# Kernel tuning notes

Hardware: AMD Instinct MI355X
Metric: run time of the kernel (lower is better)

Reference implementation:

```python
import jax, jax.numpy as jnp
import numpy as np

B, S, D, H, K = 8, 1024, 512, 512, 8  # batch, seq, input_dim, hidden, max neighbors


def setup_inputs() -> dict:
    key = jax.random.key(0)
    ks = jax.random.split(key, 10)
    p = lambda k, shape: (0.05 * jax.random.normal(k, shape, jnp.float32))
    return {
        "input_t": jax.random.normal(ks[0], (B, S, D), jnp.float32),
        "comb_idx": jax.random.randint(ks[1], (B, S, K), 0, S, jnp.int32),
        "comb_mask": jax.random.randint(ks[2], (B, S, K), 0, 2, jnp.int32),
        "order": jnp.arange(B, dtype=jnp.int64),
        # PyTorch LSTM params per direction; b = b_ih + b_hh fused (mathematically identical)
        "w_ih_f": p(ks[3], (4 * H, D)),
        "w_hh_f": p(ks[4], (4 * H, H)),
        "b_f": p(ks[5], (4 * H,)),
        "w_ih_b": p(ks[6], (4 * H, D)),
        "w_hh_b": p(ks[7], (4 * H, H)),
        "b_b": p(ks[8], (4 * H,)),
    }


def _lstm_scan(x_sbd, w_ih, w_hh, b, reverse):
    # x_sbd: [S, B, D]; PyTorch gate order i, f, g, o; zero initial state (inithidden)
    Bb = x_sbd.shape[1]
    Hh = w_hh.shape[1]
    h0 = jnp.zeros((Bb, Hh), x_sbd.dtype)
    c0 = jnp.zeros((Bb, Hh), x_sbd.dtype)

    def cell(carry, xt):
        h, c = carry
        z = xt @ w_ih.T + h @ w_hh.T + b
        i, f, g, o = jnp.split(z, 4, axis=-1)
        c = jax.nn.sigmoid(f) * c + jax.nn.sigmoid(i) * jnp.tanh(g)
        h = jax.nn.sigmoid(o) * jnp.tanh(c)
        return (h, c), h

    (hn, cn), hs = jax.lax.scan(cell, (h0, c0), x_sbd, reverse=reverse)
    return hs, hn, cn  # hs in original time order even when reverse=True


def reference(input_t, comb_idx, comb_mask, order, w_ih_f, w_hh_f, b_f, w_ih_b, w_hh_b, b_b):
    x = jnp.swapaxes(input_t, 0, 1)  # [S, B, D]
    hs_f, hn_f, cn_f = _lstm_scan(x, w_ih_f, w_hh_f, b_f, reverse=False)
    hs_b, hn_b, cn_b = _lstm_scan(x, w_ih_b, w_hh_b, b_b, reverse=True)
    padded = jnp.swapaxes(jnp.concatenate([hs_f, hs_b], axis=-1), 0, 1)  # [B, S, 2H]
    h_n = jnp.stack([hn_f, hn_b])  # [2, B, H]
    c_n = jnp.stack([cn_f, cn_b])

    # comb = batch_comb[order[idx]]
    ci = comb_idx[order]                                  # [B, S, K]
    cm = comb_mask[order].astype(padded.dtype)            # [B, S, K]
    gathered = jax.vmap(lambda xb, ib: xb[ib])(padded, ci)  # [B, S, K, 2H]
    neigh_sum = (gathered * cm[..., None]).sum(axis=2)    # [B, S, 2H]
    cnt = cm.sum(axis=-1)                                 # [B, S]
    rep = (padded + neigh_sum) / (1.0 + cnt)[..., None]   # (x_i + sum_j x_j) / (|comb_i| + 1)
    rep = rep[:, 1:-1, :]                                 # drop first/last token

    # reorder_batch_encoder_rep[order[i]] = rep[i]
    out = jnp.zeros_like(rep).at[order].set(rep)
    return out, h_n, c_n
```

## Files before the change

kernel.cpp:

```cpp
#include <hip/hip_runtime.h>
#include <stdint.h>

typedef unsigned short u16;
typedef unsigned long long u64;
typedef __attribute__((ext_vector_type(8))) short short8v;
typedef __attribute__((ext_vector_type(4))) float f32x4;

#define OUT_HN   8372224
#define OUT_CN   8380416

#define WS_FLAGS 0
#define WS_CSB   4096
#define WS_HSB0  36864
#define WS_HSB1  8433664
#define WS_ZX    16830464

__device__ __forceinline__ u16 f2bf(float f) {
  uint32_t u = __float_as_uint(f);
  u += 0x7FFFu + ((u >> 16) & 1u);
  return (u16)(u >> 16);
}
__device__ __forceinline__ float bf2f(u16 v) {
  return __uint_as_float(((uint32_t)v) << 16);
}
__device__ __forceinline__ short8v cvt8(const float* p) {
  float4 a = *(const float4*)p;
  float4 b = *(const float4*)(p + 4);
  short8v r;
  r[0] = (short)f2bf(a.x); r[1] = (short)f2bf(a.y);
  r[2] = (short)f2bf(a.z); r[3] = (short)f2bf(a.w);
  r[4] = (short)f2bf(b.x); r[5] = (short)f2bf(b.y);
  r[6] = (short)f2bf(b.z); r[7] = (short)f2bf(b.w);
  return r;
}

__global__ void k_init(uint32_t* flags) {
  if (threadIdx.x < 64) flags[threadIdx.x] = 0;
}

__global__ void k_zero(u16* h0, u16* h1, float* c) {
  int i = blockIdx.x * blockDim.x + threadIdx.x;
  if (i < 4096) { h0[i] = 0; h1[i] = 0; }
  if (i < 8192) c[i] = 0.f;
}

#define STAGE_X(tcol)                                                          \
  {                                                                            \
    _Pragma("unroll")                                                          \
    for (int half = 0; half < 2; ++half) {                                     \
      int g = tid + half * 256;                                                \
      int r = g >> 6, B = g & 63;                                              \
      const float* xr = xf + ((size_t)r * 1024 + (tcol)) * 512 + B * 8;        \
      float4 a = *(const float4*)xr;                                           \
      float4 b = *(const float4*)(xr + 4);                                     \
      short8v v;                                                               \
      v[0] = (short)f2bf(a.x); v[1] = (short)f2bf(a.y);                        \
      v[2] = (short)f2bf(a.z); v[3] = (short)f2bf(a.w);                        \
      v[4] = (short)f2bf(b.x); v[5] = (short)f2bf(b.y);                        \
      v[6] = (short)f2bf(b.z); v[7] = (short)f2bf(b.w);                        \
      *(short8v*)(xL + r * 512 + ((B ^ r) << 3)) = v;                          \
    }                                                                          \
  }

__global__ void k_zx(const float* __restrict__ xf,
                     const float* __restrict__ wihf, const float* __restrict__ wihb,
                     u16* __restrict__ zx, int s0, int seglen)
{
  const int nch  = seglen >> 5;
  const int bid  = blockIdx.x;
  const int chunk = bid % nch;
  const int wg   = (bid / nch) & 15;
  const int dir  = bid / (nch * 16);
  const int tid  = threadIdx.x;
  const int wid  = tid >> 6;
  const int lane = tid & 63;
  const int jbase = wg * 32;
  const float* wih = dir ? wihb : wihf;

  __shared__ u16 xL[8 * 512];
  __shared__ float zL[4 * 8 * 32];

  short8v bih[2][16];
  {
    const int rr = lane & 15;
    const int ko = (lane >> 4) * 8;
    #pragma unroll
    for (int nt = 0; nt < 2; ++nt) {
      const int row = wid * 512 + jbase + nt * 16 + rr;
      #pragma unroll
      for (int kt = 0; kt < 16; ++kt)
        bih[nt][kt] = cvt8(wih + (size_t)row * 512 + kt * 32 + ko);
    }
  }

  const int rB = lane & 7;
  const int q  = lane >> 4;
  const f32x4 fzero = {0.f, 0.f, 0.f, 0.f};

  for (int i = 0; i < 32; ++i) {
    const int sidx = chunk * 32 + i;
    const int gstep = s0 + sidx;
    const int tn = dir ? (1023 - gstep) : gstep;
    STAGE_X(tn);
    __syncthreads();
    f32x4 acc0 = fzero, acc1 = fzero;
    #pragma unroll
    for (int kt = 0; kt < 16; ++kt) {
      short8v ax = *(const short8v*)(xL + rB * 512 + (((kt * 4 + q) ^ rB) << 3));
      acc0 = __builtin_amdgcn_mfma_f32_16x16x32_bf16(ax, bih[0][kt], acc0, 0, 0, 0);
      acc1 = __builtin_amdgcn_mfma_f32_16x16x32_bf16(ax, bih[1][kt], acc1, 0, 0, 0);
    }
    if (lane < 32) {
      #pragma unroll
      for (int r = 0; r < 4; ++r) {
        const int brow = (lane >> 4) * 4 + r;
        zL[wid * 256 + brow * 32 + (lane & 15)]      = acc0[r];
        zL[wid * 256 + brow * 32 + 16 + (lane & 15)] = acc1[r];
      }
    }
    __syncthreads();
    if (tid < 128) {
      const int b = tid >> 4;
      const int r = (tid & 15) * 8;
      const int g = r >> 5;
      const int jj = r & 31;
      short8v v;
      #pragma unroll
      for (int w = 0; w < 8; ++w) v[w] = (short)f2bf(zL[g * 256 + b * 32 + jj + w]);
      *(short8v*)(zx + (((size_t)dir * seglen + sidx) * 16 + wg) * 1024 + tid * 8) = v;
    }
    __syncthreads();
  }
}

__launch_bounds__(256, 1)
__global__ void k_lstm(const float* __restrict__ whhf, const float* __restrict__ whhb,
                       const float* __restrict__ bias0, const float* __restrict__ bias1,
                       const u16* __restrict__ zx,
                       u16* hsb0, u16* hsb1, float* csb, float* out,
                       uint32_t* flags, int s0, int s1, int seglen)
{
  const int tid  = threadIdx.x;
  const int wid  = tid >> 6;
  const int lane = tid & 63;
  const int dir  = blockIdx.x >> 4;
  const int wg   = blockIdx.x & 15;
  const int jbase = wg * 32;

  const float* whh  = dir ? whhb : whhf;
  const float* bias = dir ? bias1 : bias0;
  u16* hsb = dir ? hsb1 : hsb0;
  uint32_t* fl = flags + dir * 16;

  __shared__ u16 hL[8 * 512];
  __shared__ float zL[4 * 8 * 32];
  __shared__ u16 hS[8 * 32];
  __shared__ u64 zxL[256];

  short8v bhh[2][16];
  {
    const int rr = lane & 15;
    const int ko = (lane >> 4) * 8;
    #pragma unroll
    for (int nt = 0; nt < 2; ++nt) {
      const int row = wid * 512 + jbase + nt * 16 + rr;
      #pragma unroll
      for (int kt = 0; kt < 16; ++kt)
        bhh[nt][kt] = cvt8(whh + (size_t)row * 512 + kt * 32 + ko);
    }
  }

  const int cb = tid >> 5;
  const int cj = tid & 31;
  const float bz0 = bias[0 * 512 + jbase + cj];
  const float bz1 = bias[1 * 512 + jbase + cj];
  const float bz2 = bias[2 * 512 + jbase + cj];
  const float bz3 = bias[3 * 512 + jbase + cj];
  float* cp = csb + dir * 4096 + cb * 512 + jbase + cj;
  float c_state = *cp;

  const int rB = lane & 7;
  const int q  = lane >> 4;
  const f32x4 fzero = {0.f, 0.f, 0.f, 0.f};
  const u16* zx16 = (const u16*)zxL;

  for (int gstep = s0; gstep < s1; ++gstep) {
    {
      const u64* zp = (const u64*)(zx + (((size_t)dir * seglen + (gstep - s0)) * 16 + wg) * 1024);
      zxL[tid] = zp[tid];
    }
    if (tid < 16) {
      int guard = 0;
      while (__hip_atomic_load(&fl[tid], __ATOMIC_RELAXED, __HIP_MEMORY_SCOPE_AGENT)
             < (uint32_t)gstep && ++guard < (1 << 15)) { }
    }
    __syncthreads();
    {
      const u64* hc = (const u64*)(hsb + (size_t)gstep * 4096);
      u64 d0 = __hip_atomic_load(hc + 4 * tid + 0, __ATOMIC_RELAXED, __HIP_MEMORY_SCOPE_AGENT);
      u64 d1 = __hip_atomic_load(hc + 4 * tid + 1, __ATOMIC_RELAXED, __HIP_MEMORY_SCOPE_AGENT);
      u64 d2 = __hip_atomic_load(hc + 4 * tid + 2, __ATOMIC_RELAXED, __HIP_MEMORY_SCOPE_AGENT);
      u64 d3 = __hip_atomic_load(hc + 4 * tid + 3, __ATOMIC_RELAXED, __HIP_MEMORY_SCOPE_AGENT);
      union { u64 qq[2]; short8v v; } p0, p1;
      p0.qq[0] = d0; p0.qq[1] = d1;
      p1.qq[0] = d2; p1.qq[1] = d3;
      int G0 = 2 * tid, G1 = 2 * tid + 1;
      int r0 = G0 >> 6, B0 = G0 & 63;
      int r1 = G1 >> 6, B1 = G1 & 63;
      *(short8v*)(hL + r0 * 512 + ((B0 ^ r0) << 3)) = p0.v;
      *(short8v*)(hL + r1 * 512 + ((B1 ^ r1) << 3)) = p1.v;
    }
    __syncthreads();
    f32x4 acc0 = fzero, acc1 = fzero;
    #pragma unroll
    for (int kt = 0; kt < 16; ++kt) {
      short8v ah = *(const short8v*)(hL + rB * 512 + (((kt * 4 + q) ^ rB) << 3));
      acc0 = __builtin_amdgcn_mfma_f32_16x16x32_bf16(ah, bhh[0][kt], acc0, 0, 0, 0);
      acc1 = __builtin_amdgcn_mfma_f32_16x16x32_bf16(ah, bhh[1][kt], acc1, 0, 0, 0);
    }
    if (lane < 32) {
      #pragma unroll
      for (int r = 0; r < 4; ++r) {
        const int brow = (lane >> 4) * 4 + r;
        zL[wid * 256 + brow * 32 + (lane & 15)]      = acc0[r];
        zL[wid * 256 + brow * 32 + 16 + (lane & 15)] = acc1[r];
      }
    }
    __syncthreads();
    {
      float zi = zL[0 * 256 + cb * 32 + cj] + bz0 + bf2f(zx16[cb * 128 +  0 + cj]);
      float zf = zL[1 * 256 + cb * 32 + cj] + bz1 + bf2f(zx16[cb * 128 + 32 + cj]);
      float zg = zL[2 * 256 + cb * 32 + cj] + bz2 + bf2f(zx16[cb * 128 + 64 + cj]);
      float zo = zL[3 * 256 + cb * 32 + cj] + bz3 + bf2f(zx16[cb * 128 + 96 + cj]);
      float si = 1.f / (1.f + __expf(-zi));
      float sf = 1.f / (1.f + __expf(-zf));
      float so = 1.f / (1.f + __expf(-zo));
      float ag = fabsf(zg); float eg = __expf(-2.f * ag);
      float tg = (1.f - eg) / (1.f + eg); tg = copysignf(tg, zg);
      c_state = sf * c_state + si * tg;
      float ac = fabsf(c_state); float ec = __expf(-2.f * ac);
      float tc = (1.f - ec) / (1.f + ec); tc = copysignf(tc, c_state);
      float h = so * tc;
      hS[cb * 32 + cj] = f2bf(h);
      if (gstep == 1023) {
        out[OUT_HN + dir * 4096 + cb * 512 + jbase + cj] = h;
        out[OUT_CN + dir * 4096 + cb * 512 + jbase + cj] = c_state;
      }
    }
    __syncthreads();
    if (tid < 64) {
      const int pb = tid >> 3;
      const int pt = tid & 7;
      u64 hv = *(const u64*)(hS + pb * 32 + 4 * pt);
      u64* dst = (u64*)(hsb + ((size_t)(gstep + 1) * 8 + pb) * 512 + jbase + 4 * pt);
      __hip_atomic_store(dst, hv, __ATOMIC_RELAXED, __HIP_MEMORY_SCOPE_AGENT);
      asm volatile("s_waitcnt vmcnt(0)" ::: "memory");
    }
    if (tid == 0) {
      __hip_atomic_store(&fl[wg], (uint32_t)(gstep + 1), __ATOMIC_RELAXED,
                         __HIP_MEMORY_SCOPE_AGENT);
    }
  }
  *cp = c_state;
}

__global__ void k_combine(const u16* __restrict__ hsb0, const u16* __restrict__ hsb1,
                          const int* __restrict__ cidx, const int* __restrict__ cmask,
                          const int* __restrict__ order, float* __restrict__ out)
{
  const int tid = threadIdx.x;
  const int b = blockIdx.x / 1022;
  const int s = 1 + (blockIdx.x % 1022);
  __shared__ int sidx[8];
  __shared__ float smask[8];
  __shared__ int rsh;
  if (tid == 0) rsh = order[b];
  __syncthreads();
  const int r = rsh;
  if (tid < 8) {
    size_t base = ((size_t)r * 1024 + s) * 8 + tid;
    sidx[tid] = cidx[base];
    smask[tid] = (float)cmask[base];
  }
  __syncthreads();
  float cnt = 0.f;
  #pragma unroll
  for (int k = 0; k < 8; ++k) cnt += smask[k];
  const float inv = 1.f / (1.f + cnt);

  const int col0 = tid * 4;
  const bool isF = col0 < 512;
  const int cloc = isF ? col0 : col0 - 512;
  const u16* hb = isF ? hsb0 : hsb1;

  float v0, v1, v2, v3;
  {
    size_t ci2 = isF ? (size_t)(s + 1) : (size_t)(1024 - s);
    ushort4 qv = *(const ushort4*)(hb + (ci2 * 8 + b) * 512 + cloc);
    v0 = bf2f(qv.x); v1 = bf2f(qv.y); v2 = bf2f(qv.z); v3 = bf2f(qv.w);
  }
  #pragma unroll
  for (int k = 0; k < 8; ++k) {
    float m = smask[k];
    if (m != 0.f) {
      int sp = sidx[k];
      size_t ci2 = isF ? (size_t)(sp + 1) : (size_t)(1024 - sp);
      ushort4 qv = *(const ushort4*)(hb + (ci2 * 8 + b) * 512 + cloc);
      v0 += m * bf2f(qv.x); v1 += m * bf2f(qv.y); v2 += m * bf2f(qv.z); v3 += m * bf2f(qv.w);
    }
  }
  size_t ob = ((size_t)r * 1022 + (s - 1)) * 1024 + col0;
  float4 ov; ov.x = v0 * inv; ov.y = v1 * inv; ov.z = v2 * inv; ov.w = v3 * inv;
  *(float4*)(out + ob) = ov;
}

extern "C" void kernel_launch(void* const* d_in, const int* in_sizes, int n_in,
                              void* d_out, int out_size, void* d_ws, size_t ws_size,
                              hipStream_t stream)
{
  const float* x      = (const float*)d_in[0];
  const int*   cidx   = (const int*)d_in[1];
  const int*   cmask  = (const int*)d_in[2];
  const int*   order  = (const int*)d_in[3];
  const float* wihf = (const float*)d_in[4];
  const float* whhf = (const float*)d_in[5];
  const float* bf   = (const float*)d_in[6];
  const float* wihb = (const float*)d_in[7];
  const float* whhb = (const float*)d_in[8];
  const float* bb   = (const float*)d_in[9];
  float* out = (float*)d_out;

  char* ws = (char*)d_ws;
  uint32_t* FLAGS = (uint32_t*)(ws + WS_FLAGS);
  float* CSB = (float*)(ws + WS_CSB);
  u16* HSB0 = (u16*)(ws + WS_HSB0);
  u16* HSB1 = (u16*)(ws + WS_HSB1);
  u16* ZX   = (u16*)(ws + WS_ZX);

  const int seglen = (ws_size >= (size_t)WS_ZX + 1024ull * 65536) ? 1024 : 128;

  hipLaunchKernelGGL(k_init, dim3(1), dim3(64), 0, stream, FLAGS);
  hipLaunchKernelGGL(k_zero, dim3(32), dim3(256), 0, stream, HSB0, HSB1, CSB);

  for (int s0 = 0; s0 < 1024; s0 += seglen) {
    hipLaunchKernelGGL(k_zx, dim3(2 * 16 * (seglen >> 5)), dim3(256), 0, stream,
                       x, wihf, wihb, ZX, s0, seglen);
    hipLaunchKernelGGL(k_lstm, dim3(32), dim3(256), 0, stream,
                       whhf, whhb, bf, bb, ZX, HSB0, HSB1, CSB, out, FLAGS,
                       s0, s0 + seglen, seglen);
  }

  hipLaunchKernelGGL(k_combine, dim3(8 * 1022), dim3(256), 0, stream,
                     HSB0, HSB1, cidx, cmask, order, out);
}
```

Baseline: 2.974 ms.

## Use a single atomic step counter and load hidden state directly into registers

Replaces the 16 per-workgroup step flags with one shared counter per direction. Each workgroup increments it after publishing its slice of h, and one thread polls until it reaches 16*gstep. The MFMA A-fragments of h are now loaded straight from global memory into registers instead of being staged through a swizzled LDS buffer, which removes one __syncthreads per step. The bf16 MFMA chain is split into even/odd accumulators for more instruction-level parallelism, and the zx prefetch and h publish are moved to different waves. The cost is atomic contention on a single counter and uncoalesced, scattered global loads of h on every step.

```diff
diff --git a/kernel.cpp b/kernel.cpp
--- a/kernel.cpp
+++ b/kernel.cpp
@@ -150,9 +150,8 @@
   const float* whh  = dir ? whhb : whhf;
   const float* bias = dir ? bias1 : bias0;
   u16* hsb = dir ? hsb1 : hsb0;
-  uint32_t* fl = flags + dir * 16;
-
-  __shared__ u16 hL[8 * 512];
+  uint32_t* cnt = flags + dir * 16;
+
   __shared__ float zL[4 * 8 * 32];
   __shared__ u16 hS[8 * 32];
   __shared__ u64 zxL[256];
@@ -185,39 +184,41 @@
   const u16* zx16 = (const u16*)zxL;
 
   for (int gstep = s0; gstep < s1; ++gstep) {
+    if (wid >= 2) {
+      const int t2 = tid - 128;
+      const u64* zp = (const u64*)(zx + (((size_t)dir * seglen + (gstep - s0)) * 16 + wg) * 1024);
+      zxL[2 * t2]     = zp[2 * t2];
+      zxL[2 * t2 + 1] = zp[2 * t2 + 1];
+    }
+    if (tid == 0) {
+      int guard = 0;
+      while (__hip_atomic_load(cnt, __ATOMIC_RELAXED, __HIP_MEMORY_SCOPE_AGENT)
+             < 16u * (uint32_t)gstep && ++guard < (1 << 16)) { }
+    }
+    __syncthreads();
+    short8v hfrag[16];
     {
-      const u64* zp = (const u64*)(zx + (((size_t)dir * seglen + (gstep - s0)) * 16 + wg) * 1024);
-      zxL[tid] = zp[tid];
-    }
-    if (tid < 16) {
-      int guard = 0;
-      while (__hip_atomic_load(&fl[tid], __ATOMIC_RELAXED, __HIP_MEMORY_SCOPE_AGENT)
-             < (uint32_t)gstep && ++guard < (1 << 15)) { }
-    }
-    __syncthreads();
-    {
-      const u64* hc = (const u64*)(hsb + (size_t)gstep * 4096);
-      u64 d0 = __hip_atomic_load(hc + 4 * tid + 0, __ATOMIC_RELAXED, __HIP_MEMORY_SCOPE_AGENT);
-      u64 d1 = __hip_atomic_load(hc + 4 * tid + 1, __ATOMIC_RELAXED, __HIP_MEMORY_SCOPE_AGENT);
-      u64 d2 = __hip_atomic_load(hc + 4 * tid + 2, __ATOMIC_RELAXED, __HIP_MEMORY_SCOPE_AGENT);
-      u64 d3 = __hip_atomic_load(hc + 4 * tid + 3, __ATOMIC_RELAXED, __HIP_MEMORY_SCOPE_AGENT);
-      union { u64 qq[2]; short8v v; } p0, p1;
-      p0.qq[0] = d0; p0.qq[1] = d1;
-      p1.qq[0] = d2; p1.qq[1] = d3;
-      int G0 = 2 * tid, G1 = 2 * tid + 1;
-      int r0 = G0 >> 6, B0 = G0 & 63;
-      int r1 = G1 >> 6, B1 = G1 & 63;
-      *(short8v*)(hL + r0 * 512 + ((B0 ^ r0) << 3)) = p0.v;
-      *(short8v*)(hL + r1 * 512 + ((B1 ^ r1) << 3)) = p1.v;
-    }
-    __syncthreads();
-    f32x4 acc0 = fzero, acc1 = fzero;
+      const char* colbase = (const char*)(hsb + (size_t)gstep * 4096);
+      #pragma unroll
+      for (int kt = 0; kt < 16; ++kt) {
+        const u64* p = (const u64*)(colbase + ((rB * 512 + kt * 32 + q * 8) * 2));
+        u64 lo = __hip_atomic_load(p,     __ATOMIC_RELAXED, __HIP_MEMORY_SCOPE_AGENT);
+        u64 hi = __hip_atomic_load(p + 1, __ATOMIC_RELAXED, __HIP_MEMORY_SCOPE_AGENT);
+        union { u64 q2[2]; short8v v; } u;
+        u.q2[0] = lo; u.q2[1] = hi;
+        hfrag[kt] = u.v;
+      }
+    }
+    f32x4 a0e = fzero, a0o = fzero, a1e = fzero, a1o = fzero;
     #pragma unroll
-    for (int kt = 0; kt < 16; ++kt) {
-      short8v ah = *(const short8v*)(hL + rB * 512 + (((kt * 4 + q) ^ rB) << 3));
-      acc0 = __builtin_amdgcn_mfma_f32_16x16x32_bf16(ah, bhh[0][kt], acc0, 0, 0, 0);
-      acc1 = __builtin_amdgcn_mfma_f32_16x16x32_bf16(ah, bhh[1][kt], acc1, 0, 0, 0);
-    }
+    for (int kt = 0; kt < 16; kt += 2) {
+      a0e = __builtin_amdgcn_mfma_f32_16x16x32_bf16(hfrag[kt],     bhh[0][kt],     a0e, 0, 0, 0);
+      a1e = __builtin_amdgcn_mfma_f32_16x16x32_bf16(hfrag[kt],     bhh[1][kt],     a1e, 0, 0, 0);
+      a0o = __builtin_amdgcn_mfma_f32_16x16x32_bf16(hfrag[kt + 1], bhh[0][kt + 1], a0o, 0, 0, 0);
+      a1o = __builtin_amdgcn_mfma_f32_16x16x32_bf16(hfrag[kt + 1], bhh[1][kt + 1], a1o, 0, 0, 0);
+    }
+    f32x4 acc0 = a0e + a0o;
+    f32x4 acc1 = a1e + a1o;
     if (lane < 32) {
       #pragma unroll
       for (int r = 0; r < 4; ++r) {
@@ -248,17 +249,16 @@
       }
     }
     __syncthreads();
-    if (tid < 64) {
-      const int pb = tid >> 3;
-      const int pt = tid & 7;
+    if (wid == 1) {
+      const int t = tid - 64;
+      const int pb = t >> 3;
+      const int pt = t & 7;
       u64 hv = *(const u64*)(hS + pb * 32 + 4 * pt);
       u64* dst = (u64*)(hsb + ((size_t)(gstep + 1) * 8 + pb) * 512 + jbase + 4 * pt);
       __hip_atomic_store(dst, hv, __ATOMIC_RELAXED, __HIP_MEMORY_SCOPE_AGENT);
       asm volatile("s_waitcnt vmcnt(0)" ::: "memory");
-    }
-    if (tid == 0) {
-      __hip_atomic_store(&fl[wg], (uint32_t)(gstep + 1), __ATOMIC_RELAXED,
-                         __HIP_MEMORY_SCOPE_AGENT);
+      if (t == 0)
+        __hip_atomic_fetch_add(cnt, 1u, __ATOMIC_RELAXED, __HIP_MEMORY_SCOPE_AGENT);
     }
   }
   *cp = c_state;
```

Result: slower. 6.151 ms (+106.8%).

## Split MFMA accumulator chains and spread per-step duties across waves

Applied to the files above, without the earlier changes.

In the recurrent LSTM step loop, the h·W_hh MFMA chain now uses two independent accumulators per output tile (even and odd k-tiles), summed at the end, which shortens the serial dependency chain on each step. The per-step load of the input-projection slice now runs on waves 2–3 only, and publishing h plus the step flag moves from wave 0 to wave 1. Wave 0 then does only the flag spin-wait, so that wait is no longer delayed by unrelated memory traffic. The cost is a few extra vector adds and a slightly different floating-point summation order.

```diff
diff --git a/kernel.cpp b/kernel.cpp
--- a/kernel.cpp
+++ b/kernel.cpp
@@ -185,9 +185,11 @@
   const u16* zx16 = (const u16*)zxL;
 
   for (int gstep = s0; gstep < s1; ++gstep) {
-    {
+    if (wid >= 2) {
+      const int t2 = tid - 128;
       const u64* zp = (const u64*)(zx + (((size_t)dir * seglen + (gstep - s0)) * 16 + wg) * 1024);
-      zxL[tid] = zp[tid];
+      zxL[2 * t2]     = zp[2 * t2];
+      zxL[2 * t2 + 1] = zp[2 * t2 + 1];
     }
     if (tid < 16) {
       int guard = 0;
@@ -211,13 +213,18 @@
       *(short8v*)(hL + r1 * 512 + ((B1 ^ r1) << 3)) = p1.v;
     }
     __syncthreads();
-    f32x4 acc0 = fzero, acc1 = fzero;
+    f32x4 a0e = fzero, a0o = fzero, a1e = fzero, a1o = fzero;
     #pragma unroll
-    for (int kt = 0; kt < 16; ++kt) {
-      short8v ah = *(const short8v*)(hL + rB * 512 + (((kt * 4 + q) ^ rB) << 3));
-      acc0 = __builtin_amdgcn_mfma_f32_16x16x32_bf16(ah, bhh[0][kt], acc0, 0, 0, 0);
-      acc1 = __builtin_amdgcn_mfma_f32_16x16x32_bf16(ah, bhh[1][kt], acc1, 0, 0, 0);
-    }
+    for (int kt = 0; kt < 16; kt += 2) {
+      short8v he = *(const short8v*)(hL + rB * 512 + ((((kt)     * 4 + q) ^ rB) << 3));
+      short8v ho = *(const short8v*)(hL + rB * 512 + ((((kt + 1) * 4 + q) ^ rB) << 3));
+      a0e = __builtin_amdgcn_mfma_f32_16x16x32_bf16(he, bhh[0][kt],     a0e, 0, 0, 0);
+      a1e = __builtin_amdgcn_mfma_f32_16x16x32_bf16(he, bhh[1][kt],     a1e, 0, 0, 0);
+      a0o = __builtin_amdgcn_mfma_f32_16x16x32_bf16(ho, bhh[0][kt + 1], a0o, 0, 0, 0);
+      a1o = __builtin_amdgcn_mfma_f32_16x16x32_bf16(ho, bhh[1][kt + 1], a1o, 0, 0, 0);
+    }
+    f32x4 acc0 = a0e + a0o;
+    f32x4 acc1 = a1e + a1o;
     if (lane < 32) {
       #pragma unroll
       for (int r = 0; r < 4; ++r) {
@@ -248,17 +255,17 @@
       }
     }
     __syncthreads();
-    if (tid < 64) {
-      const int pb = tid >> 3;
-      const int pt = tid & 7;
+    if (wid == 1) {
+      const int t = tid - 64;
+      const int pb = t >> 3;
+      const int pt = t & 7;
       u64 hv = *(const u64*)(hS + pb * 32 + 4 * pt);
       u64* dst = (u64*)(hsb + ((size_t)(gstep + 1) * 8 + pb) * 512 + jbase + 4 * pt);
       __hip_atomic_store(dst, hv, __ATOMIC_RELAXED, __HIP_MEMORY_SCOPE_AGENT);
       asm volatile("s_waitcnt vmcnt(0)" ::: "memory");
-    }
-    if (tid == 0) {
-      __hip_atomic_store(&fl[wg], (uint32_t)(gstep + 1), __ATOMIC_RELAXED,
-                         __HIP_MEMORY_SCOPE_AGENT);
+      if (t == 0)
+        __hip_atomic_store(&fl[wg], (uint32_t)(gstep + 1), __ATOMIC_RELAXED,
+                           __HIP_MEMORY_SCOPE_AGENT);
     }
   }
   *cp = c_state;
```

Result: slower. 3.198 ms (+7.5%).

## Halve LSTM recurrence workgroups to 16 with 512 threads each

Applied to the files above, without the earlier changes.

The persistent recurrent LSTM kernel now uses 8 workgroups per direction, each of 512 threads covering 64 hidden units, instead of 16 workgroups of 256 threads covering 32 units. Each step therefore has fewer cross-workgroup flags to poll and fewer participants in the global handoff of h, which targets the per-step synchronisation latency that dominates the sequential scan. In exchange each workgroup does twice the gate math per step and holds more LDS, and only 16 CUs take part in the recurrence.

```diff
diff --git a/kernel.cpp b/kernel.cpp
--- a/kernel.cpp
+++ b/kernel.cpp
@@ -133,7 +133,7 @@
   }
 }
 
-__launch_bounds__(256, 1)
+__launch_bounds__(512, 1)
 __global__ void k_lstm(const float* __restrict__ whhf, const float* __restrict__ whhb,
                        const float* __restrict__ bias0, const float* __restrict__ bias1,
                        const u16* __restrict__ zx,
@@ -143,19 +143,21 @@
   const int tid  = threadIdx.x;
   const int wid  = tid >> 6;
   const int lane = tid & 63;
-  const int dir  = blockIdx.x >> 4;
-  const int wg   = blockIdx.x & 15;
-  const int jbase = wg * 32;
+  const int dir  = blockIdx.x >> 3;
+  const int w8   = blockIdx.x & 7;
+  const int jbase = w8 * 64;
+  const int gate = wid & 3;
+  const int nh   = wid >> 2;
 
   const float* whh  = dir ? whhb : whhf;
   const float* bias = dir ? bias1 : bias0;
   u16* hsb = dir ? hsb1 : hsb0;
-  uint32_t* fl = flags + dir * 16;
+  uint32_t* fl = flags + dir * 8;
 
   __shared__ u16 hL[8 * 512];
-  __shared__ float zL[4 * 8 * 32];
-  __shared__ u16 hS[8 * 32];
-  __shared__ u64 zxL[256];
+  __shared__ float zL[4 * 8 * 64];
+  __shared__ u64 hSq[8 * 16];
+  __shared__ u64 zxL[512];
 
   short8v bhh[2][16];
   {
@@ -163,15 +165,15 @@
     const int ko = (lane >> 4) * 8;
     #pragma unroll
     for (int nt = 0; nt < 2; ++nt) {
-      const int row = wid * 512 + jbase + nt * 16 + rr;
+      const int row = gate * 512 + jbase + nh * 32 + nt * 16 + rr;
       #pragma unroll
       for (int kt = 0; kt < 16; ++kt)
         bhh[nt][kt] = cvt8(whh + (size_t)row * 512 + kt * 32 + ko);
     }
   }
 
-  const int cb = tid >> 5;
-  const int cj = tid & 31;
+  const int cb = tid >> 6;
+  const int cj = tid & 63;
   const float bz0 = bias[0 * 512 + jbase + cj];
   const float bz1 = bias[1 * 512 + jbase + cj];
   const float bz2 = bias[2 * 512 + jbase + cj];
@@ -183,13 +185,14 @@
   const int q  = lane >> 4;
   const f32x4 fzero = {0.f, 0.f, 0.f, 0.f};
   const u16* zx16 = (const u16*)zxL;
+  u16* hS = (u16*)hSq;
 
   for (int gstep = s0; gstep < s1; ++gstep) {
     {
-      const u64* zp = (const u64*)(zx + (((size_t)dir * seglen + (gstep - s0)) * 16 + wg) * 1024);
+      const u64* zp = (const u64*)(zx + (((size_t)dir * seglen + (gstep - s0)) * 16 + 2 * w8) * 1024);
       zxL[tid] = zp[tid];
     }
-    if (tid < 16) {
+    if (tid < 8) {
       int guard = 0;
       while (__hip_atomic_load(&fl[tid], __ATOMIC_RELAXED, __HIP_MEMORY_SCOPE_AGENT)
              < (uint32_t)gstep && ++guard < (1 << 15)) { }
@@ -197,18 +200,12 @@
     __syncthreads();
     {
       const u64* hc = (const u64*)(hsb + (size_t)gstep * 4096);
-      u64 d0 = __hip_atomic_load(hc + 4 * tid + 0, __ATOMIC_RELAXED, __HIP_MEMORY_SCOPE_AGENT);
-      u64 d1 = __hip_atomic_load(hc + 4 * tid + 1, __ATOMIC_RELAXED, __HIP_MEMORY_SCOPE_AGENT);
-      u64 d2 = __hip_atomic_load(hc + 4 * tid + 2, __ATOMIC_RELAXED, __HIP_MEMORY_SCOPE_AGENT);
-      u64 d3 = __hip_atomic_load(hc + 4 * tid + 3, __ATOMIC_RELAXED, __HIP_MEMORY_SCOPE_AGENT);
-      union { u64 qq[2]; short8v v; } p0, p1;
-      p0.qq[0] = d0; p0.qq[1] = d1;
-      p1.qq[0] = d2; p1.qq[1] = d3;
-      int G0 = 2 * tid, G1 = 2 * tid + 1;
-      int r0 = G0 >> 6, B0 = G0 & 63;
-      int r1 = G1 >> 6, B1 = G1 & 63;
-      *(short8v*)(hL + r0 * 512 + ((B0 ^ r0) << 3)) = p0.v;
-      *(short8v*)(hL + r1 * 512 + ((B1 ^ r1) << 3)) = p1.v;
+      u64 d0 = __hip_atomic_load(hc + 2 * tid,     __ATOMIC_RELAXED, __HIP_MEMORY_SCOPE_AGENT);
+      u64 d1 = __hip_atomic_load(hc + 2 * tid + 1, __ATOMIC_RELAXED, __HIP_MEMORY_SCOPE_AGENT);
+      union { u64 qq[2]; short8v v; } p;
+      p.qq[0] = d0; p.qq[1] = d1;
+      int r0 = tid >> 6, B0 = tid & 63;
+      *(short8v*)(hL + r0 * 512 + ((B0 ^ r0) << 3)) = p.v;
     }
     __syncthreads();
     f32x4 acc0 = fzero, acc1 = fzero;
@@ -222,16 +219,17 @@
       #pragma unroll
       for (int r = 0; r < 4; ++r) {
         const int brow = (lane >> 4) * 4 + r;
-        zL[wid * 256 + brow * 32 + (lane & 15)]      = acc0[r];
-        zL[wid * 256 + brow * 32 + 16 + (lane & 15)] = acc1[r];
+        zL[gate * 512 + brow * 64 + nh * 32 + (lane & 15)]      = acc0[r];
+        zL[gate * 512 + brow * 64 + nh * 32 + 16 + (lane & 15)] = acc1[r];
       }
     }
     __syncthreads();
     {
-      float zi = zL[0 * 256 + cb * 32 + cj] + bz0 + bf2f(zx16[cb * 128 +  0 + cj]);
-      float zf = zL[1 * 256 + cb * 32 + cj] + bz1 + bf2f(zx16[cb * 128 + 32 + cj]);
-      float zg = zL[2 * 256 + cb * 32 + cj] + bz2 + bf2f(zx16[cb * 128 + 64 + cj]);
-      float zo = zL[3 * 256 + cb * 32 + cj] + bz3 + bf2f(zx16[cb * 128 + 96 + cj]);
+      const int zo_ = (cj >> 5) * 1024 + cb * 128 + (cj & 31);
+      float zi = zL[0 * 512 + cb * 64 + cj] + bz0 + bf2f(zx16[zo_ +  0]);
+      float zf = zL[1 * 512 + cb * 64 + cj] + bz1 + bf2f(zx16[zo_ + 32]);
+      float zg = zL[2 * 512 + cb * 64 + cj] + bz2 + bf2f(zx16[zo_ + 64]);
+      float zo = zL[3 * 512 + cb * 64 + cj] + bz3 + bf2f(zx16[zo_ + 96]);
       float si = 1.f / (1.f + __expf(-zi));
       float sf = 1.f / (1.f + __expf(-zf));
       float so = 1.f / (1.f + __expf(-zo));
@@ -241,7 +239,7 @@
       float ac = fabsf(c_state); float ec = __expf(-2.f * ac);
       float tc = (1.f - ec) / (1.f + ec); tc = copysignf(tc, c_state);
       float h = so * tc;
-      hS[cb * 32 + cj] = f2bf(h);
+      hS[cb * 64 + cj] = f2bf(h);
       if (gstep == 1023) {
         out[OUT_HN + dir * 4096 + cb * 512 + jbase + cj] = h;
         out[OUT_CN + dir * 4096 + cb * 512 + jbase + cj] = c_state;
@@ -249,15 +247,19 @@
     }
     __syncthreads();
     if (tid < 64) {
-      const int pb = tid >> 3;
-      const int pt = tid & 7;
-      u64 hv = *(const u64*)(hS + pb * 32 + 4 * pt);
-      u64* dst = (u64*)(hsb + ((size_t)(gstep + 1) * 8 + pb) * 512 + jbase + 4 * pt);
-      __hip_atomic_store(dst, hv, __ATOMIC_RELAXED, __HIP_MEMORY_SCOPE_AGENT);
+      #pragma unroll
+      for (int e = 0; e < 2; ++e) {
+        const int f = 2 * tid + e;
+        const int pb = f >> 4;
+        const int pt = f & 15;
+        u64 hv = hSq[pb * 16 + pt];
+        u64* dst = (u64*)(hsb + ((size_t)(gstep + 1) * 8 + pb) * 512 + jbase + 4 * pt);
+        __hip_atomic_store(dst, hv, __ATOMIC_RELAXED, __HIP_MEMORY_SCOPE_AGENT);
+      }
       asm volatile("s_waitcnt vmcnt(0)" ::: "memory");
     }
     if (tid == 0) {
-      __hip_atomic_store(&fl[wg], (uint32_t)(gstep + 1), __ATOMIC_RELAXED,
+      __hip_atomic_store(&fl[w8], (uint32_t)(gstep + 1), __ATOMIC_RELAXED,
                          __HIP_MEMORY_SCOPE_AGENT);
     }
   }
@@ -345,7 +347,7 @@
   for (int s0 = 0; s0 < 1024; s0 += seglen) {
     hipLaunchKernelGGL(k_zx, dim3(2 * 16 * (seglen >> 5)), dim3(256), 0, stream,
                        x, wihf, wihb, ZX, s0, seglen);
-    hipLaunchKernelGGL(k_lstm, dim3(32), dim3(256), 0, stream,
+    hipLaunchKernelGGL(k_lstm, dim3(16), dim3(512), 0, stream,
                        whhf, whhb, bf, bb, ZX, HSB0, HSB1, CSB, out, FLAGS,
                        s0, s0 + seglen, seglen);
   }
```

After: 3.242 ms. +9.0%, slower.
